# Optimization experiments

Measured on AMD Instinct MI355X. Metric: run time of the kernel, lower is better.

The kernel has to match this reference:

```python
import jax, jax.numpy as jnp
import numpy as np

N_NODES = 100000
N_EDGES = 1600000
N_FEAT = 128
HIDDEN = 64
NUM_GRAPHS = 64


def setup_inputs() -> dict:
    key = jax.random.key(0)
    ks = jax.random.split(key, 10)
    x = jax.random.normal(ks[0], (N_NODES, N_FEAT), dtype=jnp.float32)
    W = jax.random.normal(ks[1], (N_FEAT, HIDDEN), dtype=jnp.float32) * (1.0 / np.sqrt(N_FEAT))
    b = jax.random.normal(ks[2], (HIDDEN,), dtype=jnp.float32) * 0.01
    W1 = jax.random.normal(ks[3], (HIDDEN, 16), dtype=jnp.float32) * (1.0 / np.sqrt(HIDDEN))
    b1 = jax.random.normal(ks[4], (16,), dtype=jnp.float32) * 0.01
    W2 = jax.random.normal(ks[5], (16, 1), dtype=jnp.float32) * 0.25
    b2 = jax.random.normal(ks[6], (1,), dtype=jnp.float32) * 0.01
    edge_index = jax.random.randint(ks[7], (2, N_EDGES), 0, N_NODES, dtype=jnp.int64)
    batch = jnp.sort(jax.random.randint(ks[8], (N_NODES,), 0, NUM_GRAPHS, dtype=jnp.int64))
    return {"x": x, "W": W, "b": b, "W1": W1, "b1": b1, "W2": W2, "b2": b2,
            "edge_index": edge_index, "batch": batch, "num_graphs": NUM_GRAPHS}


def reference(x, W, b, W1, b1, W2, b2, edge_index, batch, num_graphs):
    N = x.shape[0]
    # GCNConv: h = D^-1/2 (A + I) D^-1/2 (x W) + b
    h = x @ W  # [N, H]
    loops = jnp.arange(N, dtype=edge_index.dtype)
    src = jnp.concatenate([edge_index[0], loops])  # source nodes (with self-loops)
    dst = jnp.concatenate([edge_index[1], loops])  # target nodes
    deg = jax.ops.segment_sum(jnp.ones(dst.shape, h.dtype), dst, num_segments=N)
    dis = jnp.where(deg > 0, jax.lax.rsqrt(deg), 0.0)  # deg^-1/2, 0 for isolated
    norm = dis[src] * dis[dst]  # [E+N]
    msg = h[src] * norm[:, None]  # gather + normalize
    agg = jax.ops.segment_sum(msg, dst, num_segments=N) + b  # scatter-add + bias
    hn = jax.nn.relu(agg)
    # global_add_pool over graphs
    u = jax.ops.segment_sum(hn, batch, num_segments=num_graphs)  # [G, H]
    out = jax.nn.relu(u @ W1 + b1) @ W2 + b2  # [G, 1]
    return out.reshape(-1)
```

## Files before the change

kernel.cpp:

```cpp
#include <hip/hip_runtime.h>

#define N_NODES   100000
#define N_FEAT    128
#define N_EDGES   1600000
#define HIDDEN    64
#define NUM_GRAPHS 64
#define CHUNK   4096
#define NCHUNK  ((N_EDGES + CHUNK - 1) / CHUNK)
#define BSHIFT  8
#define NBUCKET ((N_NODES + 255) >> 8)
#define OFFS_W  (NBUCKET + 1)
#define CAP     4800
#define WT_BLOCKS 4
#define GEMM_GRID ((N_NODES + 127) / 128)

typedef unsigned int  uint32;
typedef unsigned short ushort16;

typedef __attribute__((ext_vector_type(8))) __bf16 bf16x8;
typedef __attribute__((ext_vector_type(4))) float  f32x4;
union Frag8 { bf16x8 v; unsigned short s[8]; uint4 q; };

static __device__ __forceinline__ unsigned short f2bf(float f) {
    uint32 u = __float_as_uint(f);
    u += 0x7fffu + ((u >> 16) & 1u);
    return (unsigned short)(u >> 16);
}

__global__ __launch_bounds__(512) void k_pre(const float* __restrict__ W,
                                             ushort16* __restrict__ Wt,
                                             const int* __restrict__ ei,
                                             int* __restrict__ src_out,
                                             unsigned char* __restrict__ dst8,
                                             int* __restrict__ offs) {
    __shared__ int hist[512];
    __shared__ int excl[512];
    __shared__ int ssrc[CHUNK];
    __shared__ int sdst[CHUNK];

    if (blockIdx.x < WT_BLOCKS) {
        const int base = blockIdx.x * 2048 + threadIdx.x;
#pragma unroll
        for (int j = 0; j < 4; ++j) {
            const int idx = base + j * 512;
            const int k = idx >> 6, n = idx & 63;
            Wt[n * N_FEAT + k] = f2bf(W[idx]);
        }
        return;
    }

    const int c = blockIdx.x - WT_BLOCKS;
    const int base = c * CHUNK;
    const int n = min(CHUNK, N_EDGES - base);
    const int t = threadIdx.x;
    hist[t] = 0;
    __syncthreads();

    int es[CHUNK / 512], ed[CHUNK / 512], rk[CHUNK / 512];
#pragma unroll
    for (int k = 0; k < CHUNK / 512; ++k) {
        const int i = t + k * 512;
        if (i < n) {
            ed[k] = __builtin_nontemporal_load(&ei[N_EDGES + base + i]);
            es[k] = __builtin_nontemporal_load(&ei[base + i]);
            rk[k] = atomicAdd(&hist[ed[k] >> BSHIFT], 1);
        }
    }
    __syncthreads();

    const int cnt = hist[t];
    for (int off = 1; off < 512; off <<= 1) {
        const int v = (t >= off) ? hist[t - off] : 0;
        __syncthreads();
        hist[t] += v;
        __syncthreads();
    }
    excl[t] = hist[t] - cnt;
    __syncthreads();
    if (t <= NBUCKET) offs[c * OFFS_W + t] = base + excl[t];

#pragma unroll
    for (int k = 0; k < CHUNK / 512; ++k) {
        const int i = t + k * 512;
        if (i < n) {
            const int pos = excl[ed[k] >> BSHIFT] + rk[k];
            ssrc[pos] = es[k];
            sdst[pos] = ed[k];
        }
    }
    __syncthreads();

    for (int i = t; i < n; i += 512)
        src_out[base + i] = ssrc[i];
    for (int i = t * 4; i < n; i += 2048) {
        const uint32 p = (uint32)(sdst[i] & 255)
                       | ((uint32)(sdst[i + 1] & 255) << 8)
                       | ((uint32)(sdst[i + 2] & 255) << 16)
                       | ((uint32)(sdst[i + 3] & 255) << 24);
        *(uint32*)&dst8[base + i] = p;
    }
}

__global__ __launch_bounds__(512) void k_mid(const float* __restrict__ x,
                                             const ushort16* __restrict__ Wt,
                                             ushort16* __restrict__ hb,
                                             const int* __restrict__ offs,
                                             const int* __restrict__ src_tmp,
                                             const unsigned char* __restrict__ dst8,
                                             int* __restrict__ srcs,
                                             int* __restrict__ row_ptr,
                                             int* __restrict__ row_end,
                                             float* __restrict__ dis) {
    __shared__ int hist[256];
    __shared__ int nxt[256];
    __shared__ int segb[NCHUNK];
    __shared__ int pre[NCHUNK + 1];
    __shared__ int sc[512];
    __shared__ int ssrc[CAP];
    __shared__ int sb;

    if (blockIdx.x >= NBUCKET) {
        const int t    = threadIdx.x;
        const int lane = t & 63;
        const int wv   = t >> 6;
        const int m15  = lane & 15;
        const int quad = lane >> 4;
        const int base = (blockIdx.x - NBUCKET) * 128 + wv * 16;
        const int arow = min(base + m15, N_NODES - 1);

        const float* xr = &x[(size_t)arow * N_FEAT + quad * 8];
        float4 xa[4][2];
#pragma unroll
        for (int kc = 0; kc < 4; ++kc) {
            xa[kc][0] = *(const float4*)&xr[kc * 32];
            xa[kc][1] = *(const float4*)&xr[kc * 32 + 4];
        }

        Frag8 bf[4][4];
#pragma unroll
        for (int nt = 0; nt < 4; ++nt) {
            const ushort16* wr = &Wt[(nt * 16 + m15) * N_FEAT + quad * 8];
#pragma unroll
            for (int kc = 0; kc < 4; ++kc)
                bf[nt][kc].q = *(const uint4*)&wr[kc * 32];
        }

        Frag8 af[4];
#pragma unroll
        for (int kc = 0; kc < 4; ++kc) {
            const float* f = (const float*)&xa[kc][0];
#pragma unroll
            for (int j = 0; j < 8; ++j) af[kc].s[j] = f2bf(f[j]);
        }

        f32x4 acc[4];
#pragma unroll
        for (int nt = 0; nt < 4; ++nt) acc[nt] = (f32x4){0.f, 0.f, 0.f, 0.f};

#pragma unroll
        for (int kc = 0; kc < 4; ++kc)
#pragma unroll
            for (int nt = 0; nt < 4; ++nt)
                acc[nt] = __builtin_amdgcn_mfma_f32_16x16x32_bf16(af[kc].v, bf[nt][kc].v,
                                                                  acc[nt], 0, 0, 0);

#pragma unroll
        for (int r = 0; r < 4; ++r) {
            const int orow = base + quad * 4 + r;
            if (orow < N_NODES) {
#pragma unroll
                for (int nt = 0; nt < 4; ++nt)
                    hb[(size_t)orow * HIDDEN + nt * 16 + m15] = f2bf(acc[nt][r]);
            }
        }
        return;
    }

    const int b = blockIdx.x;
    const int lo = b << BSHIFT;
    const int t = threadIdx.x;

    if (t < 256) hist[t] = 0;
    if (t == 0) sb = 0;
    __syncthreads();

    int len = 0;
    if (t < NCHUNK) {
        const int s0 = offs[t * OFFS_W + b];
        const int s1 = offs[t * OFFS_W + b + 1];
        segb[t] = s0;
        len = s1 - s0;
        atomicAdd(&sb, s0 - t * CHUNK);
    }
    sc[t] = len;
    __syncthreads();
    for (int off = 1; off < 512; off <<= 1) {
        const int v = (t >= off) ? sc[t - off] : 0;
        __syncthreads();
        sc[t] += v;
        __syncthreads();
    }
    if (t == 0) pre[0] = 0;
    if (t < NCHUNK) pre[t + 1] = sc[t];
    __syncthreads();

    const int total  = pre[NCHUNK];
    const int bstart = sb;
    const bool fits  = (total <= CAP);

    int es[(CAP + 511) / 512], ed[(CAP + 511) / 512], rk[(CAP + 511) / 512];
    int ne = 0;
    if (fits) {
        for (int e = t; e < total; e += 512) {
            int l2 = 0, h2 = NCHUNK;
            while (h2 - l2 > 1) { const int mid = (l2 + h2) >> 1;
                                  if (pre[mid] <= e) l2 = mid; else h2 = mid; }
            const int gidx = segb[l2] + (e - pre[l2]);
            const int d = dst8[gidx];
            const int s = src_tmp[gidx];
            es[ne] = s; ed[ne] = d;
            rk[ne] = atomicAdd(&hist[d], 1);
            ++ne;
        }
    } else {
        const int lane = t & 63, wv = t >> 6;
        for (int c = wv; c < NCHUNK; c += 8)
            for (int i = segb[c] + lane; i < segb[c] + (pre[c + 1] - pre[c]); i += 64)
                atomicAdd(&hist[dst8[i]], 1);
    }
    __syncthreads();

    const int cnt = (t < 256) ? hist[t] : 0;
    for (int off = 1; off < 256; off <<= 1) {
        int v = 0;
        if (t < 256 && t >= off) v = hist[t - off];
        __syncthreads();
        if (t < 256) hist[t] += v;
        __syncthreads();
    }
    if (t < 256) {
        const int excl = hist[t] - cnt;
        nxt[t] = excl;
        const int node = lo + t;
        if (node < N_NODES) {
            row_ptr[node] = bstart + excl;
            row_end[node] = bstart + excl + cnt;
            dis[node]     = rsqrtf((float)cnt + 1.0f);
        }
    }
    __syncthreads();

    if (fits) {
        for (int k = 0; k < ne; ++k)
            ssrc[nxt[ed[k]] + rk[k]] = es[k];
        __syncthreads();
        for (int i = t; i < total; i += 512)
            srcs[bstart + i] = ssrc[i];
    } else {
        const int lane = t & 63, wv = t >> 6;
        for (int c = wv; c < NCHUNK; c += 8)
            for (int i = segb[c] + lane; i < segb[c] + (pre[c + 1] - pre[c]); i += 64) {
                const int d = dst8[i];
                const int pos = atomicAdd(&nxt[d], 1);
                srcs[bstart + pos] = src_tmp[i];
            }
    }
}

__global__ __launch_bounds__(256) void k_scale(ushort16* __restrict__ hb,
                                               const float* __restrict__ dis) {
    const int i = blockIdx.x * 256 + threadIdx.x;
    const float dn = dis[i >> 3];
    uint4 v = *(const uint4*)&hb[(size_t)i * 8];
    uint4 r;
    r.x = (uint32)f2bf(__uint_as_float(v.x << 16) * dn)
        | ((uint32)f2bf(__uint_as_float(v.x & 0xffff0000u) * dn) << 16);
    r.y = (uint32)f2bf(__uint_as_float(v.y << 16) * dn)
        | ((uint32)f2bf(__uint_as_float(v.y & 0xffff0000u) * dn) << 16);
    r.z = (uint32)f2bf(__uint_as_float(v.z << 16) * dn)
        | ((uint32)f2bf(__uint_as_float(v.z & 0xffff0000u) * dn) << 16);
    r.w = (uint32)f2bf(__uint_as_float(v.w << 16) * dn)
        | ((uint32)f2bf(__uint_as_float(v.w & 0xffff0000u) * dn) << 16);
    *(uint4*)&hb[(size_t)i * 8] = r;
}

__global__ __launch_bounds__(256) void agg_kernel(const int* __restrict__ row_ptr,
                                                  const int* __restrict__ row_end,
                                                  const int* __restrict__ srcs,
                                                  const ushort16* __restrict__ hb,
                                                  const float* __restrict__ dis,
                                                  const float* __restrict__ bias,
                                                  const int* __restrict__ batch,
                                                  float* __restrict__ u) {
    __shared__ float sp[32][HIDDEN + 1];
    __shared__ int gbs[32];
    const int t = threadIdx.x;
    const int lane = t & 63;
    const int wv = t >> 6;
    const int g = lane >> 3;
    const int k = lane & 7;
    const int kb = lane & 56;
    const int base = blockIdx.x * 32;
    const int node = base + wv * 8 + g;
    const int beg = row_ptr[node];
    const int end = row_end[node];
    const int deg = end - beg;
    const float dn = dis[node];

    float acc[8];
#pragma unroll
    for (int j = 0; j < 8; ++j) acc[j] = 0.f;

    int pidx = max(min(beg + k, end - 1), 0);
    int s8 = srcs[pidx];

    for (int i0 = 0; i0 < deg; i0 += 8) {
        const int rem = deg - i0;
        const int cur = s8;
        if (i0 + 8 < deg)
            s8 = srcs[min(beg + i0 + 8 + k, end - 1)];

        int si[8];
#pragma unroll
        for (int j = 0; j < 8; ++j) si[j] = __shfl(cur, kb | j);
        uint4 v[8];
#pragma unroll
        for (int j = 0; j < 8; ++j)
            v[j] = *(const uint4*)&hb[(size_t)si[j] * HIDDEN + k * 8];
#pragma unroll
        for (int j = 0; j < 8; ++j) {
            const float m = (j < rem) ? 1.f : 0.f;
            acc[0] = fmaf(__uint_as_float(v[j].x << 16),         m, acc[0]);
            acc[1] = fmaf(__uint_as_float(v[j].x & 0xffff0000u), m, acc[1]);
            acc[2] = fmaf(__uint_as_float(v[j].y << 16),         m, acc[2]);
            acc[3] = fmaf(__uint_as_float(v[j].y & 0xffff0000u), m, acc[3]);
            acc[4] = fmaf(__uint_as_float(v[j].z << 16),         m, acc[4]);
            acc[5] = fmaf(__uint_as_float(v[j].z & 0xffff0000u), m, acc[5]);
            acc[6] = fmaf(__uint_as_float(v[j].w << 16),         m, acc[6]);
            acc[7] = fmaf(__uint_as_float(v[j].w & 0xffff0000u), m, acc[7]);
        }
    }

    {
        const uint4 hv = *(const uint4*)&hb[(size_t)node * HIDDEN + k * 8];
        const float4 b0 = *(const float4*)&bias[k * 8];
        const float4 b1 = *(const float4*)&bias[k * 8 + 4];
        float4 r0, r1;
        r0.x = fmaxf(fmaf(acc[0] + __uint_as_float(hv.x << 16),         dn, b0.x), 0.f);
        r0.y = fmaxf(fmaf(acc[1] + __uint_as_float(hv.x & 0xffff0000u), dn, b0.y), 0.f);
        r0.z = fmaxf(fmaf(acc[2] + __uint_as_float(hv.y << 16),         dn, b0.z), 0.f);
        r0.w = fmaxf(fmaf(acc[3] + __uint_as_float(hv.y & 0xffff0000u), dn, b0.w), 0.f);
        r1.x = fmaxf(fmaf(acc[4] + __uint_as_float(hv.z << 16),         dn, b1.x), 0.f);
        r1.y = fmaxf(fmaf(acc[5] + __uint_as_float(hv.z & 0xffff0000u), dn, b1.y), 0.f);
        r1.z = fmaxf(fmaf(acc[6] + __uint_as_float(hv.w << 16),         dn, b1.z), 0.f);
        r1.w = fmaxf(fmaf(acc[7] + __uint_as_float(hv.w & 0xffff0000u), dn, b1.w), 0.f);
        *(float4*)&sp[wv * 8 + g][k * 8]     = r0;
        *(float4*)&sp[wv * 8 + g][k * 8 + 4] = r1;
    }
    if (t < 32) gbs[t] = batch[base + t];
    __syncthreads();

    if (t < 64) {
        float a = sp[0][t];
        int cg = gbs[0];
        for (int r = 1; r < 32; ++r) {
            const int gr = gbs[r];
            const float vv = sp[r][t];
            if (gr == cg) a += vv;
            else { atomicAdd(&u[cg * HIDDEN + t], a); cg = gr; a = vv; }
        }
        atomicAdd(&u[cg * HIDDEN + t], a);
    }
}

__global__ __launch_bounds__(64) void mlp_kernel(const float* __restrict__ u,
                                                 const float* __restrict__ W1,
                                                 const float* __restrict__ b1,
                                                 const float* __restrict__ W2,
                                                 const float* __restrict__ b2,
                                                 float* __restrict__ out) {
    __shared__ float W1s[HIDDEN * 16];
    __shared__ float W2s[16];
    __shared__ float b1s[16];
    const int t = threadIdx.x;
    for (int i = t; i < HIDDEN * 16; i += 64) W1s[i] = W1[i];
    if (t < 16) { W2s[t] = W2[t]; b1s[t] = b1[t]; }
    __syncthreads();
    if (t < NUM_GRAPHS) {
        float uu[HIDDEN];
#pragma unroll
        for (int k = 0; k < HIDDEN; ++k) uu[k] = u[t * HIDDEN + k];
        float o = b2[0];
#pragma unroll
        for (int j = 0; j < 16; ++j) {
            float s = b1s[j];
#pragma unroll
            for (int k = 0; k < HIDDEN; ++k) s = fmaf(uu[k], W1s[k * 16 + j], s);
            o = fmaf(fmaxf(s, 0.f), W2s[j], o);
        }
        out[t] = o;
    }
}

extern "C" void kernel_launch(void* const* d_in, const int* in_sizes, int n_in,
                              void* d_out, int out_size, void* d_ws, size_t ws_size,
                              hipStream_t stream) {
    const float* x  = (const float*)d_in[0];
    const float* W  = (const float*)d_in[1];
    const float* b  = (const float*)d_in[2];
    const float* W1 = (const float*)d_in[3];
    const float* b1 = (const float*)d_in[4];
    const float* W2 = (const float*)d_in[5];
    const float* b2 = (const float*)d_in[6];
    const int*   ei = (const int*)d_in[7];
    const int* batch = (const int*)d_in[8];
    float* out = (float*)d_out;

    ushort16* hb       = (ushort16*)d_ws;
    int*      src_tmp  = (int*)(hb + (size_t)N_NODES * HIDDEN);
    unsigned char* dst8 = (unsigned char*)(src_tmp + N_EDGES);
    int*      srcs     = (int*)(dst8 + N_EDGES);
    int*      offs     = srcs + N_EDGES;
    int*      row_ptr  = offs + NCHUNK * OFFS_W;
    int*      row_end  = row_ptr + N_NODES;
    float*    dis      = (float*)(row_end + N_NODES);
    float*    u        = dis + N_NODES;
    ushort16* Wtg      = (ushort16*)(u + NUM_GRAPHS * HIDDEN);

    hipMemsetAsync(u, 0, NUM_GRAPHS * HIDDEN * sizeof(float), stream);

    k_pre<<<WT_BLOCKS + NCHUNK, 512, 0, stream>>>(W, Wtg, ei, src_tmp, dst8, offs);
    k_mid<<<NBUCKET + GEMM_GRID, 512, 0, stream>>>(x, Wtg, hb, offs, src_tmp, dst8,
                                                   srcs, row_ptr, row_end, dis);
    k_scale<<<3125, 256, 0, stream>>>(hb, dis);
    agg_kernel<<<N_NODES / 32, 256, 0, stream>>>(row_ptr, row_end, srcs, hb, dis, b, batch, u);
    mlp_kernel<<<1, 64, 0, stream>>>(u, W1, b1, W2, b2, out);
}
```

Baseline: 175.4 us.

## Fold source-degree scaling into aggregation and drop the separate scale kernel

Removes the k_scale pass that pre-multiplied hb by deg^-1/2. The aggregation instead gathers dis[src] per edge and applies it in the FMA, with the self-loop term scaled explicitly. The aggregation kernel is restructured to 256-node buckets per 512-thread block, four nodes per 8-lane group, and a segmented pooling reduction over two 128-node halves in shared memory. This saves a full read-write pass over hb and one launch, at the cost of an extra dependent gather of dis per edge, fewer and larger blocks (391), and more serialised per-group node work.

```diff
diff --git a/kernel.cpp b/kernel.cpp
--- a/kernel.cpp
+++ b/kernel.cpp
@@ -11,6 +11,7 @@
 #define NBUCKET ((N_NODES + 255) >> 8)
 #define OFFS_W  (NBUCKET + 1)
 #define CAP     4800
+#define QE      ((CAP + 511) / 512)
 #define WT_BLOCKS 4
 #define GEMM_GRID ((N_NODES + 127) / 128)
 
@@ -101,7 +102,7 @@
     }
 }
 
-__global__ __launch_bounds__(512) void k_mid(const float* __restrict__ x,
+__global__ __launch_bounds__(512) void k_mix(const float* __restrict__ x,
                                              const ushort16* __restrict__ Wt,
                                              ushort16* __restrict__ hb,
                                              const int* __restrict__ offs,
@@ -136,13 +137,13 @@
             xa[kc][1] = *(const float4*)&xr[kc * 32 + 4];
         }
 
-        Frag8 bf[4][4];
+        Frag8 bfr[4][4];
 #pragma unroll
         for (int nt = 0; nt < 4; ++nt) {
             const ushort16* wr = &Wt[(nt * 16 + m15) * N_FEAT + quad * 8];
 #pragma unroll
             for (int kc = 0; kc < 4; ++kc)
-                bf[nt][kc].q = *(const uint4*)&wr[kc * 32];
+                bfr[nt][kc].q = *(const uint4*)&wr[kc * 32];
         }
 
         Frag8 af[4];
@@ -161,7 +162,7 @@
         for (int kc = 0; kc < 4; ++kc)
 #pragma unroll
             for (int nt = 0; nt < 4; ++nt)
-                acc[nt] = __builtin_amdgcn_mfma_f32_16x16x32_bf16(af[kc].v, bf[nt][kc].v,
+                acc[nt] = __builtin_amdgcn_mfma_f32_16x16x32_bf16(af[kc].v, bfr[nt][kc].v,
                                                                   acc[nt], 0, 0, 0);
 
 #pragma unroll
@@ -208,7 +209,7 @@
     const int bstart = sb;
     const bool fits  = (total <= CAP);
 
-    int es[(CAP + 511) / 512], ed[(CAP + 511) / 512], rk[(CAP + 511) / 512];
+    int es[QE], ed[QE], rk[QE];
     int ne = 0;
     if (fits) {
         for (int e = t; e < total; e += 512) {
@@ -267,109 +268,123 @@
     }
 }
 
-__global__ __launch_bounds__(256) void k_scale(ushort16* __restrict__ hb,
-                                               const float* __restrict__ dis) {
-    const int i = blockIdx.x * 256 + threadIdx.x;
-    const float dn = dis[i >> 3];
-    uint4 v = *(const uint4*)&hb[(size_t)i * 8];
-    uint4 r;
-    r.x = (uint32)f2bf(__uint_as_float(v.x << 16) * dn)
-        | ((uint32)f2bf(__uint_as_float(v.x & 0xffff0000u) * dn) << 16);
-    r.y = (uint32)f2bf(__uint_as_float(v.y << 16) * dn)
-        | ((uint32)f2bf(__uint_as_float(v.y & 0xffff0000u) * dn) << 16);
-    r.z = (uint32)f2bf(__uint_as_float(v.z << 16) * dn)
-        | ((uint32)f2bf(__uint_as_float(v.z & 0xffff0000u) * dn) << 16);
-    r.w = (uint32)f2bf(__uint_as_float(v.w << 16) * dn)
-        | ((uint32)f2bf(__uint_as_float(v.w & 0xffff0000u) * dn) << 16);
-    *(uint4*)&hb[(size_t)i * 8] = r;
-}
-
-__global__ __launch_bounds__(256) void agg_kernel(const int* __restrict__ row_ptr,
-                                                  const int* __restrict__ row_end,
-                                                  const int* __restrict__ srcs,
-                                                  const ushort16* __restrict__ hb,
-                                                  const float* __restrict__ dis,
-                                                  const float* __restrict__ bias,
-                                                  const int* __restrict__ batch,
-                                                  float* __restrict__ u) {
-    __shared__ float sp[32][HIDDEN + 1];
-    __shared__ int gbs[32];
-    const int t = threadIdx.x;
+__global__ __launch_bounds__(512) void k_agg(const int* __restrict__ rp_g,
+                                             const int* __restrict__ re_g,
+                                             const int* __restrict__ srcs,
+                                             const ushort16* __restrict__ hb,
+                                             const float* __restrict__ dis,
+                                             const float* __restrict__ bias,
+                                             const int* __restrict__ batch,
+                                             float* __restrict__ u) {
+    __shared__ float sp[128 * 65];
+    __shared__ int   rp[256];
+    __shared__ int   rc[256];
+    __shared__ float sdn[256];
+    __shared__ int   gbs[256];
+    const int b  = blockIdx.x;
+    const int lo = b << BSHIFT;
+    const int t  = threadIdx.x;
+
+    if (t < 256) {
+        const int node = lo + t;
+        const bool ok = node < N_NODES;
+        const int p = ok ? rp_g[node] : 0;
+        rp[t]  = p;
+        rc[t]  = ok ? (re_g[node] - p) : 0;
+        sdn[t] = ok ? dis[node] : 0.f;
+        gbs[t] = ok ? batch[node] : 0;
+    }
+    __syncthreads();
+
     const int lane = t & 63;
-    const int wv = t >> 6;
-    const int g = lane >> 3;
-    const int k = lane & 7;
-    const int kb = lane & 56;
-    const int base = blockIdx.x * 32;
-    const int node = base + wv * 8 + g;
-    const int beg = row_ptr[node];
-    const int end = row_end[node];
-    const int deg = end - beg;
-    const float dn = dis[node];
-
-    float acc[8];
-#pragma unroll
-    for (int j = 0; j < 8; ++j) acc[j] = 0.f;
-
-    int pidx = max(min(beg + k, end - 1), 0);
-    int s8 = srcs[pidx];
-
-    for (int i0 = 0; i0 < deg; i0 += 8) {
-        const int rem = deg - i0;
-        const int cur = s8;
-        if (i0 + 8 < deg)
-            s8 = srcs[min(beg + i0 + 8 + k, end - 1)];
-
-        int si[8];
-#pragma unroll
-        for (int j = 0; j < 8; ++j) si[j] = __shfl(cur, kb | j);
-        uint4 v[8];
-#pragma unroll
-        for (int j = 0; j < 8; ++j)
-            v[j] = *(const uint4*)&hb[(size_t)si[j] * HIDDEN + k * 8];
-#pragma unroll
-        for (int j = 0; j < 8; ++j) {
-            const float m = (j < rem) ? 1.f : 0.f;
-            acc[0] = fmaf(__uint_as_float(v[j].x << 16),         m, acc[0]);
-            acc[1] = fmaf(__uint_as_float(v[j].x & 0xffff0000u), m, acc[1]);
-            acc[2] = fmaf(__uint_as_float(v[j].y << 16),         m, acc[2]);
-            acc[3] = fmaf(__uint_as_float(v[j].y & 0xffff0000u), m, acc[3]);
-            acc[4] = fmaf(__uint_as_float(v[j].z << 16),         m, acc[4]);
-            acc[5] = fmaf(__uint_as_float(v[j].z & 0xffff0000u), m, acc[5]);
-            acc[6] = fmaf(__uint_as_float(v[j].w << 16),         m, acc[6]);
-            acc[7] = fmaf(__uint_as_float(v[j].w & 0xffff0000u), m, acc[7]);
-        }
-    }
-
-    {
-        const uint4 hv = *(const uint4*)&hb[(size_t)node * HIDDEN + k * 8];
-        const float4 b0 = *(const float4*)&bias[k * 8];
-        const float4 b1 = *(const float4*)&bias[k * 8 + 4];
-        float4 r0, r1;
-        r0.x = fmaxf(fmaf(acc[0] + __uint_as_float(hv.x << 16),         dn, b0.x), 0.f);
-        r0.y = fmaxf(fmaf(acc[1] + __uint_as_float(hv.x & 0xffff0000u), dn, b0.y), 0.f);
-        r0.z = fmaxf(fmaf(acc[2] + __uint_as_float(hv.y << 16),         dn, b0.z), 0.f);
-        r0.w = fmaxf(fmaf(acc[3] + __uint_as_float(hv.y & 0xffff0000u), dn, b0.w), 0.f);
-        r1.x = fmaxf(fmaf(acc[4] + __uint_as_float(hv.z << 16),         dn, b1.x), 0.f);
-        r1.y = fmaxf(fmaf(acc[5] + __uint_as_float(hv.z & 0xffff0000u), dn, b1.y), 0.f);
-        r1.z = fmaxf(fmaf(acc[6] + __uint_as_float(hv.w << 16),         dn, b1.z), 0.f);
-        r1.w = fmaxf(fmaf(acc[7] + __uint_as_float(hv.w & 0xffff0000u), dn, b1.w), 0.f);
-        *(float4*)&sp[wv * 8 + g][k * 8]     = r0;
-        *(float4*)&sp[wv * 8 + g][k * 8 + 4] = r1;
-    }
-    if (t < 32) gbs[t] = batch[base + t];
-    __syncthreads();
-
-    if (t < 64) {
-        float a = sp[0][t];
-        int cg = gbs[0];
-        for (int r = 1; r < 32; ++r) {
-            const int gr = gbs[r];
-            const float vv = sp[r][t];
-            if (gr == cg) a += vv;
-            else { atomicAdd(&u[cg * HIDDEN + t], a); cg = gr; a = vv; }
-        }
-        atomicAdd(&u[cg * HIDDEN + t], a);
+    const int k    = lane & 7;
+    const int kb   = lane & 56;
+    const int grp  = (t >> 6) * 8 + (lane >> 3);
+
+    float acc[4][8];
+#pragma unroll
+    for (int a = 0; a < 4; ++a)
+#pragma unroll
+        for (int j = 0; j < 8; ++j) acc[a][j] = 0.f;
+
+#pragma unroll
+    for (int a = 0; a < 4; ++a) {
+        const int n   = grp * 4 + a;
+        const int beg = rp[n];
+        const int L   = rc[n];
+        for (int i = 0; i < L; i += 8) {
+            const int idx = beg + min(i + k, L - 1);
+            const int sv  = srcs[idx];
+            const float wv_ = dis[sv];
+            uint4 v[8];
+            float w[8];
+#pragma unroll
+            for (int j = 0; j < 8; ++j) {
+                const int sj = __shfl(sv, kb | j);
+                w[j] = __shfl(wv_, kb | j);
+                v[j] = *(const uint4*)&hb[(size_t)sj * HIDDEN + k * 8];
+            }
+            const int rem = L - i;
+#pragma unroll
+            for (int j = 0; j < 8; ++j) {
+                const float m = (j < rem) ? w[j] : 0.f;
+                acc[a][0] = fmaf(__uint_as_float(v[j].x << 16),         m, acc[a][0]);
+                acc[a][1] = fmaf(__uint_as_float(v[j].x & 0xffff0000u), m, acc[a][1]);
+                acc[a][2] = fmaf(__uint_as_float(v[j].y << 16),         m, acc[a][2]);
+                acc[a][3] = fmaf(__uint_as_float(v[j].y & 0xffff0000u), m, acc[a][3]);
+                acc[a][4] = fmaf(__uint_as_float(v[j].z << 16),         m, acc[a][4]);
+                acc[a][5] = fmaf(__uint_as_float(v[j].z & 0xffff0000u), m, acc[a][5]);
+                acc[a][6] = fmaf(__uint_as_float(v[j].w << 16),         m, acc[a][6]);
+                acc[a][7] = fmaf(__uint_as_float(v[j].w & 0xffff0000u), m, acc[a][7]);
+            }
+        }
+    }
+
+    const float4 b0 = *(const float4*)&bias[k * 8];
+    const float4 b1 = *(const float4*)&bias[k * 8 + 4];
+    const int f   = t & 63;
+    const int seg = t >> 6;
+
+    for (int h = 0; h < 2; ++h) {
+        if ((grp >> 5) == h) {
+#pragma unroll
+            for (int a = 0; a < 4; ++a) {
+                const int n = grp * 4 + a;
+                const int nl = n - h * 128;
+                const uint4 hv = *(const uint4*)
+                    &hb[(size_t)min(lo + n, N_NODES - 1) * HIDDEN + k * 8];
+                const float dn = sdn[n];
+                float4 r0, r1;
+                r0.x = fmaxf(fmaf(fmaf(__uint_as_float(hv.x << 16),         dn, acc[a][0]), dn, b0.x), 0.f);
+                r0.y = fmaxf(fmaf(fmaf(__uint_as_float(hv.x & 0xffff0000u), dn, acc[a][1]), dn, b0.y), 0.f);
+                r0.z = fmaxf(fmaf(fmaf(__uint_as_float(hv.y << 16),         dn, acc[a][2]), dn, b0.z), 0.f);
+                r0.w = fmaxf(fmaf(fmaf(__uint_as_float(hv.y & 0xffff0000u), dn, acc[a][3]), dn, b0.w), 0.f);
+                r1.x = fmaxf(fmaf(fmaf(__uint_as_float(hv.z << 16),         dn, acc[a][4]), dn, b1.x), 0.f);
+                r1.y = fmaxf(fmaf(fmaf(__uint_as_float(hv.z & 0xffff0000u), dn, acc[a][5]), dn, b1.y), 0.f);
+                r1.z = fmaxf(fmaf(fmaf(__uint_as_float(hv.w << 16),         dn, acc[a][6]), dn, b1.z), 0.f);
+                r1.w = fmaxf(fmaf(fmaf(__uint_as_float(hv.w & 0xffff0000u), dn, acc[a][7]), dn, b1.w), 0.f);
+                *(float4*)&sp[nl * 65 + k * 8]     = r0;
+                *(float4*)&sp[nl * 65 + k * 8 + 4] = r1;
+            }
+        }
+        __syncthreads();
+
+        float a_ = 0.f;
+        int   cg = -1;
+        for (int n2 = seg * 16; n2 < seg * 16 + 16; ++n2) {
+            const int node = lo + h * 128 + n2;
+            if (node >= N_NODES) break;
+            const float r = sp[n2 * 65 + f];
+            const int gr = gbs[h * 128 + n2];
+            if (gr != cg) {
+                if (cg >= 0) atomicAdd(&u[cg * HIDDEN + f], a_);
+                cg = gr; a_ = r;
+            } else {
+                a_ += r;
+            }
+        }
+        if (cg >= 0) atomicAdd(&u[cg * HIDDEN + f], a_);
+        __syncthreads();
     }
 }
 
@@ -430,9 +445,8 @@
     hipMemsetAsync(u, 0, NUM_GRAPHS * HIDDEN * sizeof(float), stream);
 
     k_pre<<<WT_BLOCKS + NCHUNK, 512, 0, stream>>>(W, Wtg, ei, src_tmp, dst8, offs);
-    k_mid<<<NBUCKET + GEMM_GRID, 512, 0, stream>>>(x, Wtg, hb, offs, src_tmp, dst8,
+    k_mix<<<NBUCKET + GEMM_GRID, 512, 0, stream>>>(x, Wtg, hb, offs, src_tmp, dst8,
                                                    srcs, row_ptr, row_end, dis);
-    k_scale<<<3125, 256, 0, stream>>>(hb, dis);
-    agg_kernel<<<N_NODES / 32, 256, 0, stream>>>(row_ptr, row_end, srcs, hb, dis, b, batch, u);
+    k_agg<<<NBUCKET, 512, 0, stream>>>(row_ptr, row_end, srcs, hb, dis, b, batch, u);
     mlp_kernel<<<1, 64, 0, stream>>>(u, W1, b1, W2, b2, out);
 }
```

After: 191.7 us. 9.3% more time.
